# Kernel tuning notes

Measured on AMD Instinct MI355X. Metric: run time of the kernel, lower is better.

Reference implementation:

```python
import jax, jax.numpy as jnp
import numpy as np

N_NODES = 50000
N_EDGES = 1600000
IN_CH = 128
OUT_CH = 128


def setup_inputs() -> dict:
    key = jax.random.key(0)
    k1, k2, k3, k4, k5 = jax.random.split(key, 5)
    x = jax.random.normal(k1, (N_NODES, IN_CH), dtype=jnp.float32)
    # edge_index[0] = destination (row), edge_index[1] = source (col)
    edge_index = jax.random.randint(k2, (2, N_EDGES), 0, N_NODES, dtype=jnp.int64)
    # Linear parameters (PyTorch default init: U(-1/sqrt(fan_in), 1/sqrt(fan_in)))
    bound = 1.0 / np.sqrt(IN_CH)
    W = jax.random.uniform(k3, (OUT_CH, IN_CH), dtype=jnp.float32, minval=-bound, maxval=bound)
    b = jax.random.uniform(k4, (OUT_CH,), dtype=jnp.float32, minval=-bound, maxval=bound)
    return {"x": x, "edge_index": edge_index, "W": W, "b": b}


def reference(x, edge_index, W, b) -> jnp.ndarray:
    # Linear projection: h = x @ W^T + b  -> [N, OUT_CH]
    h = jnp.einsum("nd,od->no", x, W) + b
    # spmm sum aggregation: out[dst] = sum_{edges e: dst(e)=dst} h[src(e)]
    dst = edge_index[0]
    src = edge_index[1]
    out = jax.ops.segment_sum(h[src], dst, num_segments=N_NODES)
    return out
```

## Files before the change

kernel.cpp:

```cpp
#include <hip/hip_runtime.h>

constexpr int N  = 50000;
constexpr int E  = 1600000;
constexpr int CH = 128;

constexpr int BSZ  = 32;
constexpr int NB   = (N + BSZ - 1) / BSZ;
constexpr int CAP  = 1280;
constexpr int SRTCAP = CAP + BSZ * 31 + 64;
constexpr int PBLK = 320;
constexpr int EPB  = E / PBLK;
constexpr int CPT  = (NB + 255) / 256;
constexpr int GEMM_BLOCKS = N / 16;

constexpr size_t H_OFF     = 0;
constexpr size_t H_SZ      = (size_t)(N + 1) * CH * 2;
constexpr size_t PAIRS_OFF = H_OFF + H_SZ;
constexpr size_t PAIRS_SZ  = (size_t)NB * CAP * 4;
constexpr size_t GCUR_OFF  = PAIRS_OFF + PAIRS_SZ;
constexpr size_t GCUR_SZ   = 6400;
constexpr size_t REQUIRED  = GCUR_OFF + GCUR_SZ;
constexpr size_t FB_REQUIRED = H_SZ;

static __device__ __forceinline__ ushort f2bf(float f) {
    unsigned u = __float_as_uint(f);
    return (ushort)((u + 0x7fffu + ((u >> 16) & 1u)) >> 16);
}
static __device__ __forceinline__ float bf_lo(unsigned u) { return __uint_as_float(u << 16); }
static __device__ __forceinline__ float bf_hi(unsigned u) { return __uint_as_float(u & 0xffff0000u); }

typedef __attribute__((ext_vector_type(8))) short bf16x8;
typedef __attribute__((ext_vector_type(4))) float f32x4;

static __device__ __forceinline__ void gemm_body(int gb, int tid,
                                                 const float* __restrict__ x,
                                                 const float* __restrict__ W,
                                                 const float* __restrict__ bias,
                                                 ushort* __restrict__ h) {
    const int m    = tid & 15;
    const int q    = (tid >> 4) & 3;
    const int wave = tid >> 6;
    const int r0   = gb * 16;
    const int c0   = wave * 32;

    const float* xrow = x + (size_t)(r0 + m) * CH + q * 8;
    const float* wr0  = W + (size_t)(c0 + m) * CH + q * 8;
    const float* wr1  = wr0 + 16 * CH;

    f32x4 acc0 = {0.f, 0.f, 0.f, 0.f};
    f32x4 acc1 = {0.f, 0.f, 0.f, 0.f};

#pragma unroll
    for (int kc = 0; kc < CH; kc += 32) {
        float4 xa = *(const float4*)(xrow + kc);
        float4 xb = *(const float4*)(xrow + kc + 4);
        float4 wa0 = *(const float4*)(wr0 + kc);
        float4 wb0 = *(const float4*)(wr0 + kc + 4);
        float4 wa1 = *(const float4*)(wr1 + kc);
        float4 wb1 = *(const float4*)(wr1 + kc + 4);
        bf16x8 a, b0, b1;
        a[0] = (short)f2bf(xa.x); a[1] = (short)f2bf(xa.y);
        a[2] = (short)f2bf(xa.z); a[3] = (short)f2bf(xa.w);
        a[4] = (short)f2bf(xb.x); a[5] = (short)f2bf(xb.y);
        a[6] = (short)f2bf(xb.z); a[7] = (short)f2bf(xb.w);
        b0[0] = (short)f2bf(wa0.x); b0[1] = (short)f2bf(wa0.y);
        b0[2] = (short)f2bf(wa0.z); b0[3] = (short)f2bf(wa0.w);
        b0[4] = (short)f2bf(wb0.x); b0[5] = (short)f2bf(wb0.y);
        b0[6] = (short)f2bf(wb0.z); b0[7] = (short)f2bf(wb0.w);
        b1[0] = (short)f2bf(wa1.x); b1[1] = (short)f2bf(wa1.y);
        b1[2] = (short)f2bf(wa1.z); b1[3] = (short)f2bf(wa1.w);
        b1[4] = (short)f2bf(wb1.x); b1[5] = (short)f2bf(wb1.y);
        b1[6] = (short)f2bf(wb1.z); b1[7] = (short)f2bf(wb1.w);
        acc0 = __builtin_amdgcn_mfma_f32_16x16x32_bf16(a, b0, acc0, 0, 0, 0);
        acc1 = __builtin_amdgcn_mfma_f32_16x16x32_bf16(a, b1, acc1, 0, 0, 0);
    }

    const int col0 = c0 + m;
    const float bb0 = bias[col0];
    const float bb1 = bias[col0 + 16];
#pragma unroll
    for (int r = 0; r < 4; r++) {
        size_t row = (size_t)(r0 + q * 4 + r) * CH;
        h[row + col0]      = f2bf(acc0[r] + bb0);
        h[row + col0 + 16] = f2bf(acc1[r] + bb1);
    }
}

__global__ __launch_bounds__(256) void gemm_and_scatter(const float* __restrict__ x,
                                                        const float* __restrict__ W,
                                                        const float* __restrict__ bias,
                                                        ushort* __restrict__ h,
                                                        const int* __restrict__ ei,
                                                        int* __restrict__ gcur,
                                                        unsigned* __restrict__ pairs) {
    __shared__ unsigned srt32[EPB];
    __shared__ int cnt[NB];
    __shared__ int delta[NB];
    __shared__ int wsum[4];
    const int bid = blockIdx.x;
    const int tid = threadIdx.x;

    if (bid >= PBLK) {
        gemm_body(bid - PBLK, tid, x, W, bias, h);
        return;
    }

    const int k = bid;
    const int* dp = ei + k * EPB;
    const int* sp = ei + E + k * EPB;

    if (bid == 0 && tid < 64) ((unsigned*)(h + (size_t)N * CH))[tid] = 0u;

    for (int j = tid; j < NB; j += 256) cnt[j] = 0;
    __syncthreads();
    for (int i = tid; i < EPB; i += 256) atomicAdd(&cnt[dp[i] >> 5], 1);
    __syncthreads();

    for (int j = tid; j < NB; j += 256) {
        int c = cnt[j];
        delta[j] = j * CAP + (c ? atomicAdd(&gcur[j], c) : 0);
    }

    {
        const int base = tid * CPT;
        int cv[CPT];
        int s = 0;
#pragma unroll
        for (int i = 0; i < CPT; i++) {
            int j = base + i;
            cv[i] = (j < NB) ? cnt[j] : 0;
            s += cv[i];
        }
        const int lane = tid & 63;
        const int wid  = tid >> 6;
        int incl = s;
#pragma unroll
        for (int o = 1; o < 64; o <<= 1) {
            int u = __shfl_up(incl, o);
            if (lane >= o) incl += u;
        }
        if (lane == 63) wsum[wid] = incl;
        __syncthreads();
        int run = incl - s;
        for (int w = 0; w < wid; w++) run += wsum[w];
#pragma unroll
        for (int i = 0; i < CPT; i++) {
            int j = base + i;
            if (j < NB) { cnt[j] = run; delta[j] -= run; }
            run += cv[i];
        }
    }
    __syncthreads();

    for (int i = tid; i < EPB; i += 256) {
        int d = dp[i], s = sp[i];
        int bkt = d >> 5;
        unsigned w = ((unsigned)bkt << 21) | ((unsigned)(d & (BSZ - 1)) << 16) | (unsigned)s;
        int p = atomicAdd(&cnt[bkt], 1);
        srt32[p] = w;
    }
    __syncthreads();

    for (int i = tid; i < EPB; i += 256) {
        unsigned w = srt32[i];
        int bkt = w >> 21;
        int gdst = delta[bkt] + i;
        if (gdst < (bkt + 1) * CAP)
            pairs[gdst] = w;
    }
}

#define ACC8(v) do { \
    a0 += bf_lo((v).x); a1 += bf_hi((v).x); a2 += bf_lo((v).y); a3 += bf_hi((v).y); \
    a4 += bf_lo((v).z); a5 += bf_hi((v).z); a6 += bf_lo((v).w); a7 += bf_hi((v).w); } while (0)

__global__ __launch_bounds__(512)
void agg_fused(const ushort* __restrict__ h,
               const unsigned* __restrict__ pairs,
               const int* __restrict__ gcur,
               float* __restrict__ out) {
    __shared__ unsigned raw[CAP];
    __shared__ ushort   srt[SRTCAP];
    __shared__ int hist[BSZ], offs[BSZ], cur[BSZ], cpad[BSZ];
    const int b = blockIdx.x, t = threadIdx.x;
    const int cnt = min(gcur[b], CAP);
    const int wave = t >> 6;
    const int lane = t & 63;
    const int quarter = lane >> 4;
    const int cq      = lane & 15;

    if (t < BSZ) hist[t] = 0;
    __syncthreads();

    const unsigned* slab = pairs + (size_t)b * CAP;
    for (int i = t; i < cnt; i += 512) {
        unsigned w = slab[i];
        raw[i] = w;
        atomicAdd(&hist[(w >> 16) & (BSZ - 1)], 1);
    }
    __syncthreads();

    if (t < BSZ) {
        int c  = hist[t];
        int cp = (c + 31) & ~31;
        int incl = cp;
#pragma unroll
        for (int o = 1; o < BSZ; o <<= 1) {
            int u = __shfl_up(incl, o);
            if (lane >= o) incl += u;
        }
        offs[t] = incl - cp;
        cur[t]  = incl - cp;
        cpad[t] = cp;
    }
    __syncthreads();

    const int tot = offs[BSZ - 1] + cpad[BSZ - 1];
    const int fill = min(tot + 32, SRTCAP);
    for (int i = t; i < fill; i += 512) srt[i] = (ushort)N;
    __syncthreads();
    for (int i = t; i < cnt; i += 512) {
        unsigned w = raw[i];
        int p = atomicAdd(&cur[(w >> 16) & (BSZ - 1)], 1);
        srt[p] = (ushort)(w & 0xffffu);
    }
    __syncthreads();

    const ushort* hp = h + (size_t)cq * 8;

#pragma unroll 1
    for (int j = 0; j < 4; j++) {
        const int nl = wave * 4 + j;
        const int st = offs[nl];
        const int cp = cpad[nl];
        float a0 = 0.f, a1 = 0.f, a2 = 0.f, a3 = 0.f;
        float a4 = 0.f, a5 = 0.f, a6 = 0.f, a7 = 0.f;
        int base = st + quarter;
        int sA0 = srt[base], sA1 = srt[base + 4], sA2 = srt[base + 8], sA3 = srt[base + 12];
        uint4 vA0 = *(const uint4*)(hp + (size_t)sA0 * CH);
        uint4 vA1 = *(const uint4*)(hp + (size_t)sA1 * CH);
        uint4 vA2 = *(const uint4*)(hp + (size_t)sA2 * CH);
        uint4 vA3 = *(const uint4*)(hp + (size_t)sA3 * CH);
#pragma unroll 1
        for (int i = 0; i < cp; i += 32) {
            int sB0 = srt[base + 16], sB1 = srt[base + 20], sB2 = srt[base + 24], sB3 = srt[base + 28];
            uint4 vB0 = *(const uint4*)(hp + (size_t)sB0 * CH);
            uint4 vB1 = *(const uint4*)(hp + (size_t)sB1 * CH);
            uint4 vB2 = *(const uint4*)(hp + (size_t)sB2 * CH);
            uint4 vB3 = *(const uint4*)(hp + (size_t)sB3 * CH);
            ACC8(vA0); ACC8(vA1); ACC8(vA2); ACC8(vA3);
            const int nb = base + ((i + 32 < cp) ? 32 : 0);
            sA0 = srt[nb]; sA1 = srt[nb + 4]; sA2 = srt[nb + 8]; sA3 = srt[nb + 12];
            vA0 = *(const uint4*)(hp + (size_t)sA0 * CH);
            vA1 = *(const uint4*)(hp + (size_t)sA1 * CH);
            vA2 = *(const uint4*)(hp + (size_t)sA2 * CH);
            vA3 = *(const uint4*)(hp + (size_t)sA3 * CH);
            ACC8(vB0); ACC8(vB1); ACC8(vB2); ACC8(vB3);
            base += 32;
        }
        a0 += __shfl_xor(a0, 16); a0 += __shfl_xor(a0, 32);
        a1 += __shfl_xor(a1, 16); a1 += __shfl_xor(a1, 32);
        a2 += __shfl_xor(a2, 16); a2 += __shfl_xor(a2, 32);
        a3 += __shfl_xor(a3, 16); a3 += __shfl_xor(a3, 32);
        a4 += __shfl_xor(a4, 16); a4 += __shfl_xor(a4, 32);
        a5 += __shfl_xor(a5, 16); a5 += __shfl_xor(a5, 32);
        a6 += __shfl_xor(a6, 16); a6 += __shfl_xor(a6, 32);
        a7 += __shfl_xor(a7, 16); a7 += __shfl_xor(a7, 32);
        const int n = b * BSZ + nl;
        if (quarter == 0 && n < N) {
            float* op = out + (size_t)n * CH + cq * 8;
            *(float4*)(op)     = make_float4(a0, a1, a2, a3);
            *(float4*)(op + 4) = make_float4(a4, a5, a6, a7);
        }
    }
}

__global__ __launch_bounds__(256) void gemm_only(const float* __restrict__ x,
                                                 const float* __restrict__ W,
                                                 const float* __restrict__ bias,
                                                 ushort* __restrict__ h) {
    gemm_body(blockIdx.x, threadIdx.x, x, W, bias, h);
}

__global__ void atomic_agg(const ushort* __restrict__ h, const int* __restrict__ ei,
                           float* __restrict__ out) {
    int tid = blockIdx.x * blockDim.x + threadIdx.x;
    int e  = tid >> 5;
    int cg = (tid & 31) * 4;
    if (e < E) {
        int d = ei[e];
        int s = ei[E + e];
        ushort4 v = *(const ushort4*)(h + (size_t)s * CH + cg);
        float* o = out + (size_t)d * CH + cg;
        atomicAdd(o + 0, __uint_as_float((unsigned)v.x << 16));
        atomicAdd(o + 1, __uint_as_float((unsigned)v.y << 16));
        atomicAdd(o + 2, __uint_as_float((unsigned)v.z << 16));
        atomicAdd(o + 3, __uint_as_float((unsigned)v.w << 16));
    }
}

extern "C" void kernel_launch(void* const* d_in, const int* in_sizes, int n_in,
                              void* d_out, int out_size, void* d_ws, size_t ws_size,
                              hipStream_t stream) {
    const float* x  = (const float*)d_in[0];
    const int*   ei = (const int*)d_in[1];
    const float* W  = (const float*)d_in[2];
    const float* b  = (const float*)d_in[3];
    float* out = (float*)d_out;

    char* ws = (char*)d_ws;
    ushort* h = (ushort*)(ws + H_OFF);

    if (ws_size >= REQUIRED) {
        unsigned* pairs = (unsigned*)(ws + PAIRS_OFF);
        int*      gcur  = (int*)(ws + GCUR_OFF);

        hipMemsetAsync(gcur, 0, NB * sizeof(int), stream);
        gemm_and_scatter<<<PBLK + GEMM_BLOCKS, 256, 0, stream>>>(x, W, b, h, ei, gcur, pairs);
        agg_fused<<<NB, 512, 0, stream>>>(h, pairs, gcur, out);
    } else if (ws_size >= FB_REQUIRED) {
        gemm_only<<<GEMM_BLOCKS, 256, 0, stream>>>(x, W, b, h);
        hipMemsetAsync(out, 0, (size_t)out_size * sizeof(float), stream);
        int total = E * 32;
        atomic_agg<<<(total + 255) / 256, 256, 0, stream>>>(h, ei, out);
    }
}
```

Baseline: 179.3 us.

## Replace block-local counting sort with direct global atomic bucket scatter

Removes the shared-memory histogram, prefix-scan and local sort stage in the scatter blocks. Each thread now claims a slot in its destination bucket with a global atomic on a padded counter (one counter per 64 bytes) and writes the packed pair directly. The scatter work is merged into every GEMM block instead of using separate scatter blocks. This drops several block barriers and the large LDS footprint, but issues 1.6M global atomics, which contend on hot buckets and lose the locality of the sorted writes.

```diff
diff --git a/kernel.cpp b/kernel.cpp
--- a/kernel.cpp
+++ b/kernel.cpp
@@ -8,17 +8,16 @@
 constexpr int NB   = (N + BSZ - 1) / BSZ;
 constexpr int CAP  = 1280;
 constexpr int SRTCAP = CAP + BSZ * 31 + 64;
-constexpr int PBLK = 320;
-constexpr int EPB  = E / PBLK;
-constexpr int CPT  = (NB + 255) / 256;
 constexpr int GEMM_BLOCKS = N / 16;
+constexpr int EPB  = E / GEMM_BLOCKS;
+constexpr int GSTRIDE = 16;
 
 constexpr size_t H_OFF     = 0;
 constexpr size_t H_SZ      = (size_t)(N + 1) * CH * 2;
 constexpr size_t PAIRS_OFF = H_OFF + H_SZ;
 constexpr size_t PAIRS_SZ  = (size_t)NB * CAP * 4;
 constexpr size_t GCUR_OFF  = PAIRS_OFF + PAIRS_SZ;
-constexpr size_t GCUR_SZ   = 6400;
+constexpr size_t GCUR_SZ   = (size_t)NB * GSTRIDE * 4;
 constexpr size_t REQUIRED  = GCUR_OFF + GCUR_SZ;
 constexpr size_t FB_REQUIRED = H_SZ;
 
@@ -93,81 +92,23 @@
                                                         const int* __restrict__ ei,
                                                         int* __restrict__ gcur,
                                                         unsigned* __restrict__ pairs) {
-    __shared__ unsigned srt32[EPB];
-    __shared__ int cnt[NB];
-    __shared__ int delta[NB];
-    __shared__ int wsum[4];
     const int bid = blockIdx.x;
     const int tid = threadIdx.x;
 
-    if (bid >= PBLK) {
-        gemm_body(bid - PBLK, tid, x, W, bias, h);
-        return;
-    }
-
-    const int k = bid;
-    const int* dp = ei + k * EPB;
-    const int* sp = ei + E + k * EPB;
-
     if (bid == 0 && tid < 64) ((unsigned*)(h + (size_t)N * CH))[tid] = 0u;
 
-    for (int j = tid; j < NB; j += 256) cnt[j] = 0;
-    __syncthreads();
-    for (int i = tid; i < EPB; i += 256) atomicAdd(&cnt[dp[i] >> 5], 1);
-    __syncthreads();
-
-    for (int j = tid; j < NB; j += 256) {
-        int c = cnt[j];
-        delta[j] = j * CAP + (c ? atomicAdd(&gcur[j], c) : 0);
-    }
-
-    {
-        const int base = tid * CPT;
-        int cv[CPT];
-        int s = 0;
-#pragma unroll
-        for (int i = 0; i < CPT; i++) {
-            int j = base + i;
-            cv[i] = (j < NB) ? cnt[j] : 0;
-            s += cv[i];
-        }
-        const int lane = tid & 63;
-        const int wid  = tid >> 6;
-        int incl = s;
-#pragma unroll
-        for (int o = 1; o < 64; o <<= 1) {
-            int u = __shfl_up(incl, o);
-            if (lane >= o) incl += u;
-        }
-        if (lane == 63) wsum[wid] = incl;
-        __syncthreads();
-        int run = incl - s;
-        for (int w = 0; w < wid; w++) run += wsum[w];
-#pragma unroll
-        for (int i = 0; i < CPT; i++) {
-            int j = base + i;
-            if (j < NB) { cnt[j] = run; delta[j] -= run; }
-            run += cv[i];
-        }
-    }
-    __syncthreads();
-
-    for (int i = tid; i < EPB; i += 256) {
-        int d = dp[i], s = sp[i];
+    const int e0 = bid * EPB + tid;
+#pragma unroll
+    for (int r = 0; r < EPB / 256; r++) {
+        const int e = e0 + r * 256;
+        int d = ei[e], s = ei[E + e];
         int bkt = d >> 5;
         unsigned w = ((unsigned)bkt << 21) | ((unsigned)(d & (BSZ - 1)) << 16) | (unsigned)s;
-        int p = atomicAdd(&cnt[bkt], 1);
-        srt32[p] = w;
-    }
-    __syncthreads();
-
-    for (int i = tid; i < EPB; i += 256) {
-        unsigned w = srt32[i];
-        int bkt = w >> 21;
-        int gdst = delta[bkt] + i;
-        if (gdst < (bkt + 1) * CAP)
-            pairs[gdst] = w;
-    }
+        int pos = atomicAdd(&gcur[bkt * GSTRIDE], 1);
+        if (pos < CAP) pairs[bkt * CAP + pos] = w;
+    }
+
+    gemm_body(bid, tid, x, W, bias, h);
 }
 
 #define ACC8(v) do { \
@@ -183,7 +124,7 @@
     __shared__ ushort   srt[SRTCAP];
     __shared__ int hist[BSZ], offs[BSZ], cur[BSZ], cpad[BSZ];
     const int b = blockIdx.x, t = threadIdx.x;
-    const int cnt = min(gcur[b], CAP);
+    const int cnt = min(gcur[b * GSTRIDE], CAP);
     const int wave = t >> 6;
     const int lane = t & 63;
     const int quarter = lane >> 4;
@@ -315,8 +256,8 @@
         unsigned* pairs = (unsigned*)(ws + PAIRS_OFF);
         int*      gcur  = (int*)(ws + GCUR_OFF);
 
-        hipMemsetAsync(gcur, 0, NB * sizeof(int), stream);
-        gemm_and_scatter<<<PBLK + GEMM_BLOCKS, 256, 0, stream>>>(x, W, b, h, ei, gcur, pairs);
+        hipMemsetAsync(gcur, 0, GCUR_SZ, stream);
+        gemm_and_scatter<<<GEMM_BLOCKS, 256, 0, stream>>>(x, W, b, h, ei, gcur, pairs);
         agg_fused<<<NB, 512, 0, stream>>>(h, pairs, gcur, out);
     } else if (ws_size >= FB_REQUIRED) {
         gemm_only<<<GEMM_BLOCKS, 256, 0, stream>>>(x, W, b, h);
```

Measured after the change: 227.7 us. 27.0% more time.
